# Optimization experiments

Measured on AMD Instinct MI355X. Metric: run time of the kernel, lower is better.

The kernel has to match this reference:

```python
import jax, jax.numpy as jnp
from jax import lax
import numpy as np

N_DYADIC = 0      # dyadic refinement parameter `n` of the original module
N_CHUNKS = 2      # `n_chunks` of the original module


def _solve_sig_kernel(Z, n):
    """Explicit finite-difference solve of the signature-kernel Goursat PDE
    for k(Z, Z). Z: (A, L, D). Scheme (as in sig_kernel_batch, implicit=False):
        K[i+1, j+1] = K[i+1, j] + K[i, j+1] + K[i, j] * (<dz_i, dz_j> - 1)
    on a dyadically refined grid of size (2^n*(L-1)+1)^2. Returns K[:, -1, -1].
    """
    two_n = 2 ** n
    dz = Z[:, 1:, :] - Z[:, :-1, :]                      # (A, L-1, D)
    dzf = jnp.repeat(dz, two_n, axis=1) / float(two_n)   # fine increments (A, LL, D)
    inc = jnp.einsum('aid,ajd->aij', dzf, dzf)           # Gram matrix (A, LL, LL)
    A, LL, _ = inc.shape

    row0 = jnp.ones((A, LL + 1), inc.dtype)              # K[0, :] = 1

    def row_step(prev_row, inc_i):
        # prev_row: (A, LL+1) = K[i, :]; inc_i: (A, LL)
        def cell(carry, vals):
            p_up, p_diag, e = vals                        # K[i,j+1], K[i,j], inc[i,j]
            new = carry + p_up + p_diag * (e - 1.0)       # carry = K[i+1,j]
            return new, new
        init = jnp.ones((A,), inc.dtype)                  # K[i+1, 0] = 1
        _, newsT = lax.scan(cell, init,
                            (prev_row[:, 1:].T, prev_row[:, :-1].T, inc_i.T))
        new_row = jnp.concatenate([init[:, None], newsT.T], axis=1)
        return new_row, None

    last_row, _ = lax.scan(row_step, row0, jnp.moveaxis(inc, 1, 0))
    return last_row[:, -1]                                # k(Z, Z), shape (A,)


def _sig_distance(x, y, n):
    # Z = cat([X, flip(Y, dim=1)], dim=1);  d = mean(sqrt(k(Z,Z) - 1))
    Z = jnp.concatenate([x, y[:, ::-1, :]], axis=1)
    k = _solve_sig_kernel(Z, n)
    return jnp.mean(jnp.sqrt(k - 1.0))


def _chunk_bounds(M, k):
    # torch.chunk(X, k, dim=1): chunks of size ceil(M/k)
    cs = -(-M // k)
    return [(i, min(i + cs, M)) for i in range(0, M, cs)]


def sig_loss(X, Y, n=N_DYADIC, n_chunks=N_CHUNKS):
    if n_chunks == 1:
        return _sig_distance(X, Y, n)
    M = X.shape[1]
    dist = jnp.zeros((), X.dtype)
    for k in range(2, n_chunks + 1):
        bx = _chunk_bounds(M, k)
        by = _chunk_bounds(Y.shape[1], k)
        for (a1, b1), (a2, b2), (c1, d1), (c2, d2) in zip(bx[:-1], bx[1:], by[:-1], by[1:]):
            x12 = jnp.concatenate([X[:, a1:b1], X[:, a2:b2]], axis=1)
            y12 = jnp.concatenate([Y[:, c1:d1], Y[:, c2:d2]], axis=1)
            dist = dist + _sig_distance(x12, y12, n)
    return dist


def setup_inputs() -> dict:
    key = jax.random.key(0)
    k1, k2 = jax.random.split(key)
    # scale 0.02 keeps path increments small so k(Z,Z) (exponential in path
    # norm) stays in fp32 range, as in real signature-kernel usage.
    X = jax.random.normal(k1, (64, 256, 8), dtype=jnp.float32) * 0.02
    Y = jax.random.normal(k2, (64, 256, 8), dtype=jnp.float32) * 0.02
    return {"X": X, "Y": Y}


def reference(X, Y):
    return sig_loss(X, Y)
```

## Files before the change

kernel.cpp:

```cpp
#include <hip/hip_runtime.h>
#include <math.h>

#define AA    64
#define SEQ   256
#define LL    511
#define MPAD  320
#define CH    6
#define NCHK  54

typedef float v2f __attribute__((ext_vector_type(2)));
typedef float v4f __attribute__((ext_vector_type(4)));

__global__ void zero_out_kernel(float* out) { out[0] = 0.0f; }

__device__ __forceinline__ float wave_shr1(float x, float fill) {
    int r = __builtin_amdgcn_update_dpp(__float_as_int(fill), __float_as_int(x),
                                        0x138, 0xF, 0xF, false);
    return __int_as_float(r);
}

__device__ __forceinline__ const float* zptr(const float* __restrict__ X,
                                             const float* __restrict__ Y,
                                             int a, int p) {
    return (p < SEQ) ? (X + ((size_t)a * SEQ + p) * 8)
                     : (Y + ((size_t)a * SEQ + (LL - p)) * 8);
}
__device__ __forceinline__ void zload(const float* p, v2f z[4]) {
    float4 u = reinterpret_cast<const float4*>(p)[0];
    float4 v = reinterpret_cast<const float4*>(p)[1];
    z[0].x = u.x; z[0].y = u.y; z[1].x = u.z; z[1].y = u.w;
    z[2].x = v.x; z[2].y = v.y; z[3].x = v.z; z[3].y = v.w;
}

__device__ __forceinline__ void produce_m_lds(
        int t, int m, const v2f rowdz[8][4], const v2f (*dzs)[2][256],
        float* __restrict__ ebase) {
    const int pm0 = m - t;
    const bool v0 = (unsigned)pm0 < 256u;
    const bool v1 = (unsigned)pm0 < 255u;
    const int pm = pm0 < 0 ? 0 : (pm0 > 255 ? 255 : pm0);

    v2f c0[4], c1[4];
    #pragma unroll
    for (int p = 0; p < 4; ++p) {
        c0[p] = dzs[p][0][pm];
        c1[p] = dzs[p][1][pm];
    }

    union { v4f q[4]; float f[16]; } eb;
    #pragma unroll
    for (int k = 0; k < 8; ++k) {
        v2f a0 = {-0.5f, -0.5f}, a1 = {-0.5f, -0.5f};
        #pragma unroll
        for (int p = 0; p < 4; ++p) {
            a0 += rowdz[k][p] * c0[p];
            a1 += rowdz[k][p] * c1[p];
        }
        eb.f[k]     = v0 ? (a0.x + a0.y) : 0.0f;
        eb.f[8 + k] = v1 ? (a1.x + a1.y) : 0.0f;
    }
    #pragma unroll
    for (int qi = 0; qi < 4; ++qi)
        *reinterpret_cast<v4f*>(ebase + qi * 256 + t * 4) = eb.q[qi];
}

#define F0(MI, k) (Rg[MI][(k) >> 2][(k) & 3])
#define F1(MI, k) (Rg[MI][2 + ((k) >> 2)][(k) & 3])
#define PROCM(MI, m_)                                                          \
    { const int pm = (m_) - t;                                                 \
      const bool v0 = (unsigned)pm < 256u;                                     \
      const bool v1 = (unsigned)pm < 255u;                                     \
      const float sb0 = wave_shr1(bot0, 1.0f);                                 \
      const float sb1 = wave_shr1(bot1, 1.0f);                                 \
      float up = sb0, diag = nb_prev;                                          \
      _Pragma("unroll")                                                        \
      for (int k = 0; k < 8; ++k) {                                            \
          const float nv = fmaf(diag, F0(MI, k), L[k]) + up;                   \
          diag = L[k]; L[k] = v0 ? nv : L[k]; up = nv;                         \
      }                                                                        \
      bot0 = L[7];                                                             \
      up = sb1; diag = sb0;                                                    \
      _Pragma("unroll")                                                        \
      for (int k = 0; k < 8; ++k) {                                            \
          const float nv = fmaf(diag, F1(MI, k), L[k]) + up;                   \
          diag = L[k]; L[k] = v1 ? nv : L[k]; up = nv;                         \
      }                                                                        \
      bot1 = L[7];                                                             \
      nb_prev = sb1; }

__global__ __launch_bounds__(448) void fused_kernel(
        const float* __restrict__ X, const float* __restrict__ Y,
        float* __restrict__ out) {
    const int a  = blockIdx.x;
    const int wv = threadIdx.x >> 6;
    const int t  = threadIdx.x & 63;

    __shared__ __align__(16) float Ebuf[2][CH][1024];
    __shared__ __align__(16) v2f  dzs[4][2][256];

    for (int i = threadIdx.x; i < 512; i += 448) {
        v2f d[4];
        if (i < LL) {
            v2f za[4], zb[4];
            zload(zptr(X, Y, a, i),     za);
            zload(zptr(X, Y, a, i + 1), zb);
            #pragma unroll
            for (int p = 0; p < 4; ++p) d[p] = zb[p] - za[p];
        } else {
            #pragma unroll
            for (int p = 0; p < 4; ++p) { d[p].x = 0.0f; d[p].y = 0.0f; }
        }
        #pragma unroll
        for (int p = 0; p < 4; ++p) dzs[p][i & 1][i >> 1] = d[p];
    }
    __syncthreads();

    v2f rowdz[8][4];
    if (wv < CH) {
        #pragma unroll
        for (int k = 0; k < 8; ++k) {
            const int r = 8 * t + k;
            #pragma unroll
            for (int p = 0; p < 4; ++p) rowdz[k][p] = dzs[p][r & 1][r >> 1];
        }
        produce_m_lds(t, wv, rowdz, dzs, &Ebuf[0][wv][0]);
    }

    float L[8];
    #pragma unroll
    for (int k = 0; k < 8; ++k) L[k] = 1.0f;
    float bot0 = 1.0f, bot1 = 1.0f, nb_prev = 1.0f;

    __syncthreads();

    for (int c = 0; c < NCHK; ++c) {
        if (wv < CH) {
            const int cc = c + 1;
            if (cc < NCHK)
                produce_m_lds(t, cc * CH + wv, rowdz, dzs, &Ebuf[cc & 1][wv][0]);
        } else {
            const float* bp = &Ebuf[c & 1][0][0] + t * 4;
            v4f Rg[CH][4];
            #pragma unroll
            for (int mi = 0; mi < CH; ++mi)
                #pragma unroll
                for (int qi = 0; qi < 4; ++qi)
                    Rg[mi][qi] = *reinterpret_cast<const v4f*>(bp + mi * 1024 + qi * 256);
            const int mb = c * CH;
            PROCM(0, mb);     PROCM(1, mb + 1); PROCM(2, mb + 2);
            PROCM(3, mb + 3); PROCM(4, mb + 4); PROCM(5, mb + 5);
        }
        __syncthreads();
    }

    if (wv == CH && t == 63)
        atomicAdd(out, sqrtf(L[6] - 1.0f) * (1.0f / (float)AA));
}

extern "C" void kernel_launch(void* const* d_in, const int* in_sizes, int n_in,
                              void* d_out, int out_size, void* d_ws, size_t ws_size,
                              hipStream_t stream) {
    const float* X = (const float*)d_in[0];
    const float* Y = (const float*)d_in[1];
    float* out = (float*)d_out;

    zero_out_kernel<<<1, 1, 0, stream>>>(out);
    fused_kernel<<<AA, 448, 0, stream>>>(X, Y, out);
}
```

Before: 105.1 us.

## Double chunk size, branch over inactive diagonals, prioritize consumer wave

```diff
diff --git a/kernel.cpp b/kernel.cpp
--- a/kernel.cpp
+++ b/kernel.cpp
@@ -5,8 +5,8 @@
 #define SEQ   256
 #define LL    511
 #define MPAD  320
-#define CH    6
-#define NCHK  54
+#define CH    12
+#define NCHK  27
 
 typedef float v2f __attribute__((ext_vector_type(2)));
 typedef float v4f __attribute__((ext_vector_type(4)));
@@ -68,24 +68,27 @@
 #define F1(MI, k) (Rg[MI][2 + ((k) >> 2)][(k) & 3])
 #define PROCM(MI, m_)                                                          \
     { const int pm = (m_) - t;                                                 \
-      const bool v0 = (unsigned)pm < 256u;                                     \
-      const bool v1 = (unsigned)pm < 255u;                                     \
-      const float sb0 = wave_shr1(bot0, 1.0f);                                 \
-      const float sb1 = wave_shr1(bot1, 1.0f);                                 \
-      float up = sb0, diag = nb_prev;                                          \
-      _Pragma("unroll")                                                        \
-      for (int k = 0; k < 8; ++k) {                                            \
-          const float nv = fmaf(diag, F0(MI, k), L[k]) + up;                   \
-          diag = L[k]; L[k] = v0 ? nv : L[k]; up = nv;                         \
+      float sb0 = wave_shr1(bot0, 1.0f);                                       \
+      float sb1 = wave_shr1(bot1, 1.0f);                                       \
+      asm volatile("" : "+v"(sb0), "+v"(sb1));                                 \
+      if ((unsigned)pm < 256u) {                                               \
+          float up = sb0, diag = nb_prev;                                      \
+          _Pragma("unroll")                                                    \
+          for (int k = 0; k < 8; ++k) {                                        \
+              const float nv = fmaf(diag, F0(MI, k), L[k]) + up;               \
+              diag = L[k]; L[k] = nv; up = nv;                                 \
+          }                                                                    \
+          bot0 = L[7];                                                         \
+          if (pm < 255) {                                                      \
+              up = sb1; diag = sb0;                                            \
+              _Pragma("unroll")                                                \
+              for (int k = 0; k < 8; ++k) {                                    \
+                  const float nv = fmaf(diag, F1(MI, k), L[k]) + up;           \
+                  diag = L[k]; L[k] = nv; up = nv;                             \
+              }                                                                \
+              bot1 = L[7];                                                     \
+          }                                                                    \
       }                                                                        \
-      bot0 = L[7];                                                             \
-      up = sb1; diag = sb0;                                                    \
-      _Pragma("unroll")                                                        \
-      for (int k = 0; k < 8; ++k) {                                            \
-          const float nv = fmaf(diag, F1(MI, k), L[k]) + up;                   \
-          diag = L[k]; L[k] = v1 ? nv : L[k]; up = nv;                         \
-      }                                                                        \
-      bot1 = L[7];                                                             \
       nb_prev = sb1; }
 
 __global__ __launch_bounds__(448) void fused_kernel(
@@ -116,14 +119,15 @@
     __syncthreads();
 
     v2f rowdz[8][4];
-    if (wv < CH) {
+    if (wv < 6) {
         #pragma unroll
         for (int k = 0; k < 8; ++k) {
             const int r = 8 * t + k;
             #pragma unroll
             for (int p = 0; p < 4; ++p) rowdz[k][p] = dzs[p][r & 1][r >> 1];
         }
-        produce_m_lds(t, wv, rowdz, dzs, &Ebuf[0][wv][0]);
+        produce_m_lds(t, wv,     rowdz, dzs, &Ebuf[0][wv][0]);
+        produce_m_lds(t, wv + 6, rowdz, dzs, &Ebuf[0][wv + 6][0]);
     }
 
     float L[8];
@@ -131,13 +135,17 @@
     for (int k = 0; k < 8; ++k) L[k] = 1.0f;
     float bot0 = 1.0f, bot1 = 1.0f, nb_prev = 1.0f;
 
+    if (wv == 6) __builtin_amdgcn_s_setprio(1);
     __syncthreads();
 
     for (int c = 0; c < NCHK; ++c) {
-        if (wv < CH) {
+        if (wv < 6) {
             const int cc = c + 1;
-            if (cc < NCHK)
-                produce_m_lds(t, cc * CH + wv, rowdz, dzs, &Ebuf[cc & 1][wv][0]);
+            if (cc < NCHK) {
+                const int mb = cc * CH;
+                produce_m_lds(t, mb + wv,     rowdz, dzs, &Ebuf[cc & 1][wv][0]);
+                produce_m_lds(t, mb + 6 + wv, rowdz, dzs, &Ebuf[cc & 1][wv + 6][0]);
+            }
         } else {
             const float* bp = &Ebuf[c & 1][0][0] + t * 4;
             v4f Rg[CH][4];
@@ -147,13 +155,15 @@
                 for (int qi = 0; qi < 4; ++qi)
                     Rg[mi][qi] = *reinterpret_cast<const v4f*>(bp + mi * 1024 + qi * 256);
             const int mb = c * CH;
-            PROCM(0, mb);     PROCM(1, mb + 1); PROCM(2, mb + 2);
-            PROCM(3, mb + 3); PROCM(4, mb + 4); PROCM(5, mb + 5);
+            PROCM(0,  mb);      PROCM(1,  mb + 1);  PROCM(2,  mb + 2);
+            PROCM(3,  mb + 3);  PROCM(4,  mb + 4);  PROCM(5,  mb + 5);
+            PROCM(6,  mb + 6);  PROCM(7,  mb + 7);  PROCM(8,  mb + 8);
+            PROCM(9,  mb + 9);  PROCM(10, mb + 10); PROCM(11, mb + 11);
         }
         __syncthreads();
     }
 
-    if (wv == CH && t == 63)
+    if (wv == 6 && t == 63)
         atomicAdd(out, sqrtf(L[6] - 1.0f) * (1.0f / (float)AA));
 }
 
```

Result: slower. 123.2 us (+17.2%).

## Replace per-chunk block barriers with LDS counter producer-consumer ring buffer

Applied to the files above, without the earlier changes.

```diff
diff --git a/kernel.cpp b/kernel.cpp
--- a/kernel.cpp
+++ b/kernel.cpp
@@ -4,9 +4,9 @@
 #define AA    64
 #define SEQ   256
 #define LL    511
-#define MPAD  320
 #define CH    6
 #define NCHK  54
+#define NBUF  4
 
 typedef float v2f __attribute__((ext_vector_type(2)));
 typedef float v4f __attribute__((ext_vector_type(4)));
@@ -95,8 +95,10 @@
     const int wv = threadIdx.x >> 6;
     const int t  = threadIdx.x & 63;
 
-    __shared__ __align__(16) float Ebuf[2][CH][1024];
+    __shared__ __align__(16) float Ebuf[NBUF][CH][1024];
     __shared__ __align__(16) v2f  dzs[4][2][256];
+    __shared__ int prod_cnt[NBUF];
+    __shared__ int cons_cnt;
 
     for (int i = threadIdx.x; i < 512; i += 448) {
         v2f d[4];
@@ -113,33 +115,42 @@
         #pragma unroll
         for (int p = 0; p < 4; ++p) dzs[p][i & 1][i >> 1] = d[p];
     }
+    if (threadIdx.x < NBUF) prod_cnt[threadIdx.x] = 0;
+    if (threadIdx.x == NBUF) cons_cnt = 0;
     __syncthreads();
 
-    v2f rowdz[8][4];
     if (wv < CH) {
+        v2f rowdz[8][4];
         #pragma unroll
         for (int k = 0; k < 8; ++k) {
             const int r = 8 * t + k;
             #pragma unroll
             for (int p = 0; p < 4; ++p) rowdz[k][p] = dzs[p][r & 1][r >> 1];
         }
-        produce_m_lds(t, wv, rowdz, dzs, &Ebuf[0][wv][0]);
-    }
+        volatile int* vcons = &cons_cnt;
+        for (int c = 0; c < NCHK; ++c) {
+            if (c >= NBUF) {
+                while (*vcons < c - (NBUF - 1)) __builtin_amdgcn_s_sleep(2);
+            }
+            produce_m_lds(t, c * CH + wv, rowdz, dzs, &Ebuf[c & (NBUF - 1)][wv][0]);
+            asm volatile("s_waitcnt lgkmcnt(0)" ::: "memory");
+            if (t == 0) atomicAdd(&prod_cnt[c & (NBUF - 1)], 1);
+        }
+    } else {
+        __builtin_amdgcn_s_setprio(1);
+        float L[8];
+        #pragma unroll
+        for (int k = 0; k < 8; ++k) L[k] = 1.0f;
+        float bot0 = 1.0f, bot1 = 1.0f, nb_prev = 1.0f;
 
-    float L[8];
-    #pragma unroll
-    for (int k = 0; k < 8; ++k) L[k] = 1.0f;
-    float bot0 = 1.0f, bot1 = 1.0f, nb_prev = 1.0f;
+        volatile int* vp = prod_cnt;
+        for (int c = 0; c < NCHK; ++c) {
+            const int slot = c & (NBUF - 1);
+            const int need = 6 * ((c >> 2) + 1);
+            while (vp[slot] < need) __builtin_amdgcn_s_sleep(1);
+            asm volatile("s_waitcnt lgkmcnt(0)" ::: "memory");
 
-    __syncthreads();
-
-    for (int c = 0; c < NCHK; ++c) {
-        if (wv < CH) {
-            const int cc = c + 1;
-            if (cc < NCHK)
-                produce_m_lds(t, cc * CH + wv, rowdz, dzs, &Ebuf[cc & 1][wv][0]);
-        } else {
-            const float* bp = &Ebuf[c & 1][0][0] + t * 4;
+            const float* bp = &Ebuf[slot][0][0] + t * 4;
             v4f Rg[CH][4];
             #pragma unroll
             for (int mi = 0; mi < CH; ++mi)
@@ -149,12 +160,13 @@
             const int mb = c * CH;
             PROCM(0, mb);     PROCM(1, mb + 1); PROCM(2, mb + 2);
             PROCM(3, mb + 3); PROCM(4, mb + 4); PROCM(5, mb + 5);
+
+            asm volatile("s_waitcnt lgkmcnt(0)" ::: "memory");
+            if (t == 0) *((volatile int*)&cons_cnt) = c + 1;
         }
-        __syncthreads();
+
+        if (t == 63) atomicAdd(out, sqrtf(L[6] - 1.0f) * (1.0f / (float)AA));
     }
-
-    if (wv == CH && t == 63)
-        atomicAdd(out, sqrtf(L[6] - 1.0f) * (1.0f / (float)AA));
 }
 
 extern "C" void kernel_launch(void* const* d_in, const int* in_sizes, int n_in,
```

New measurement: 103.2 us. Within noise of the previous version (-1.7%).
